# Optimization experiments

Measured on AMD Instinct MI355X. Metric: run time of the kernel, lower is better.

Reference implementation:

```python
import jax, jax.numpy as jnp
import numpy as np
import math

DIM, HEADS = 512, 8
D_K = DIM // HEADS

def setup_inputs() -> dict:
    key = jax.random.key(0)
    ks = jax.random.split(key, 6)
    B, LK, LQ = 16, 2048, 256
    s = 1.0 / math.sqrt(DIM)
    return {
        "L": jax.random.normal(ks[0], (B, LK, DIM), jnp.float32),
        "G": jax.random.normal(ks[1], (B, LQ, DIM), jnp.float32),
        "Wq": jax.random.normal(ks[2], (DIM, DIM), jnp.float32) * s,
        "bq": jnp.zeros((DIM,), jnp.float32),
        "Wo": jax.random.normal(ks[3], (DIM, DIM), jnp.float32) * s,
        "bo": jnp.zeros((DIM,), jnp.float32),
    }

def reference(L, G, Wq, bq, Wo, bo):
    B = G.shape[0]
    # Q projection from global tokens; K,V are raw local features split into heads
    q = (G @ Wq + bq).reshape(B, -1, HEADS, D_K)          # [B, Lq, H, d]
    k = L.reshape(B, -1, HEADS, D_K)                      # [B, Lk, H, d]
    v = k
    # double scaling as in source: / sqrt(d_k) * dim**-0.5
    scale = (D_K ** -0.5) * (DIM ** -0.5)
    dots = jnp.einsum("bqhd,bkhd->bhqk", q, k) * scale    # [B, H, Lq, Lk]
    attn = jax.nn.softmax(dots, axis=-1)
    x = jnp.einsum("bhqk,bkhd->bqhd", attn, v)            # [B, Lq, H, d]
    x = x.reshape(B, -1, HEADS * D_K)
    return x @ Wo + bo
```

## Files before the change

kernel.cpp:

```cpp
#include <hip/hip_runtime.h>

#define KSTR 72

typedef __attribute__((ext_vector_type(8))) short short8;
typedef __attribute__((ext_vector_type(4))) float f32x4;

#define EXP2F(x) __builtin_amdgcn_exp2f(x)

__device__ __forceinline__ unsigned short f2bf(float f) {
    union { float f; unsigned u; } v; v.f = f;
    unsigned r = v.u + 0x7fff + ((v.u >> 16) & 1);
    return (unsigned short)(r >> 16);
}
__device__ __forceinline__ unsigned pk2(float a, float b) {
    return (unsigned)f2bf(a) | ((unsigned)f2bf(b) << 16);
}

__global__ __launch_bounds__(256) void conv_W(const float* __restrict__ Wq,
                                              const float* __restrict__ Wo,
                                              unsigned short* __restrict__ WqF,
                                              unsigned short* __restrict__ WoF) {
    const float* W = blockIdx.y ? Wo : Wq;
    unsigned short* WF = blockIdx.y ? WoF : WqF;
    int g = blockIdx.x * 256 + threadIdx.x;
    int lane = g & 63, ntg = (g >> 6) & 31, kt = g >> 11;
    int c = lane & 15, quad = lane >> 4;
    const float* wp = W + (size_t)(32 * kt + 8 * quad) * 512 + 16 * ntg + c;
    float v[8];
    #pragma unroll
    for (int j = 0; j < 8; j++) v[j] = wp[(size_t)j * 512];
    uint4 u;
    u.x = pk2(v[0], v[1]); u.y = pk2(v[2], v[3]);
    u.z = pk2(v[4], v[5]); u.w = pk2(v[6], v[7]);
    *(uint4*)(WF + (size_t)g * 8) = u;
}

__global__ __launch_bounds__(256) void conv_L(const float* __restrict__ Lmat,
                                              unsigned short* __restrict__ KF,
                                              unsigned short* __restrict__ VF) {
    __shared__ unsigned short KFs[4096];
    __shared__ unsigned short VFs[4096];
    const int blk = blockIdx.x;
    const int t = blk & 31, h = (blk >> 5) & 7, b = blk >> 8;
    const int tid = threadIdx.x;
    const int key = tid & 63, wv = tid >> 6;

    const float* src = Lmat + ((size_t)(b * 2048 + 64 * t + key)) * 512 + 64 * h + 16 * wv;
    float4 a0 = *(const float4*)src;
    float4 a1 = *(const float4*)(src + 4);
    float4 a2 = *(const float4*)(src + 8);
    float4 a3 = *(const float4*)(src + 12);
    float vals[16] = {a0.x, a0.y, a0.z, a0.w, a1.x, a1.y, a1.z, a1.w,
                      a2.x, a2.y, a2.z, a2.w, a3.x, a3.y, a3.z, a3.w};
    #pragma unroll
    for (int i = 0; i < 16; i++) {
        int d = 16 * wv + i;
        unsigned short bv = f2bf(vals[i]);
        KFs[((((key >> 4) * 2 + (d >> 5)) * 64) + ((d >> 3) & 3) * 16 + (key & 15)) * 8 + (d & 7)] = bv;
        VFs[((((d >> 4) * 2 + (key >> 5)) * 64) + ((key >> 3) & 3) * 16 + (d & 15)) * 8 + (key & 7)] = bv;
    }
    __syncthreads();
    size_t gbase = (size_t)blk * 4096 + tid * 16;
    *(uint4*)(KF + gbase)     = *(const uint4*)&KFs[tid * 16];
    *(uint4*)(KF + gbase + 8) = *(const uint4*)&KFs[tid * 16 + 8];
    *(uint4*)(VF + gbase)     = *(const uint4*)&VFs[tid * 16];
    *(uint4*)(VF + gbase + 8) = *(const uint4*)&VFs[tid * 16 + 8];
}

template<bool A_BF16, bool OUT_BF16>
__global__ __launch_bounds__(256, 2) void gemm_direct(const void* __restrict__ Ap,
                                                      const unsigned short* __restrict__ WF,
                                                      const float* __restrict__ bias,
                                                      void* __restrict__ Cp,
                                                      float oscale) {
    const int tid = threadIdx.x;
    const int wv = tid >> 6, lane = tid & 63;
    const int c = lane & 15, quad = lane >> 4;
    const int m0 = blockIdx.x * 64, n0 = blockIdx.y * 64;
    const int row = m0 + 16 * wv + c;

    f32x4 acc[4];
    #pragma unroll
    for (int nt = 0; nt < 4; nt++) acc[nt] = (f32x4){0.f, 0.f, 0.f, 0.f};

    #pragma unroll
    for (int kk = 0; kk < 16; kk++) {
        short8 af;
        if (A_BF16) {
            af = *(const short8*)((const unsigned short*)Ap + (size_t)row * 512 + 32 * kk + 8 * quad);
        } else {
            const float* ap = (const float*)Ap + (size_t)row * 512 + 32 * kk + 8 * quad;
            float4 x0 = *(const float4*)ap;
            float4 x1 = *(const float4*)(ap + 4);
            af[0] = (short)f2bf(x0.x); af[1] = (short)f2bf(x0.y);
            af[2] = (short)f2bf(x0.z); af[3] = (short)f2bf(x0.w);
            af[4] = (short)f2bf(x1.x); af[5] = (short)f2bf(x1.y);
            af[6] = (short)f2bf(x1.z); af[7] = (short)f2bf(x1.w);
        }
        #pragma unroll
        for (int nt = 0; nt < 4; nt++) {
            short8 bf = *(const short8*)(WF +
                (((size_t)kk * 32 + (n0 >> 4) + nt) * 64 + lane) * 8);
            acc[nt] = __builtin_amdgcn_mfma_f32_16x16x32_bf16(af, bf, acc[nt], 0, 0, 0);
        }
    }

    #pragma unroll
    for (int nt = 0; nt < 4; nt++) {
        float bv = bias[n0 + 16 * nt + c];
        #pragma unroll
        for (int r = 0; r < 4; r++) {
            float v = (acc[nt][r] + bv) * oscale;
            size_t idx = (size_t)(m0 + 16 * wv + 4 * quad + r) * 512 + n0 + 16 * nt + c;
            if (OUT_BF16) ((unsigned short*)Cp)[idx] = f2bf(v);
            else          ((float*)Cp)[idx] = v;
        }
    }
}

__global__ __launch_bounds__(256, 2) void attn_frag(const unsigned short* __restrict__ Q,
                                                    const unsigned short* __restrict__ KF,
                                                    const unsigned short* __restrict__ VF,
                                                    unsigned short* __restrict__ X) {
    __shared__ __align__(16) char shm_raw[4 * 64 * 68 * 4];
    unsigned short (*Pw)[4][16 * KSTR] = (unsigned short (*)[4][16 * KSTR])shm_raw;
    float (*Mrg)[64][68] = (float (*)[64][68])shm_raw;

    const int raw = blockIdx.x;
    const int h  = raw & 7;
    const int qt = (raw >> 3) & 3;
    const int b  = raw >> 5;
    const int tid = threadIdx.x;
    const int wv = tid >> 6, lane = tid & 63;
    const int c = lane & 15, quad = lane >> 4;

    short8 qa[4][2];
    #pragma unroll
    for (int g = 0; g < 4; g++) {
        const unsigned short* qsrc =
            Q + ((size_t)(b * 256 + qt * 64 + 16 * g + c)) * 512 + h * 64;
        qa[g][0] = *(const short8*)(qsrc + 8 * quad);
        qa[g][1] = *(const short8*)(qsrc + 32 + 8 * quad);
    }

    short8 ones;
    #pragma unroll
    for (int i = 0; i < 8; i++) ones[i] = (short)0x3F80;

    f32x4 oacc[4][4];
    #pragma unroll
    for (int g = 0; g < 4; g++)
        #pragma unroll
        for (int dt = 0; dt < 4; dt++) oacc[g][dt] = (f32x4){0.f, 0.f, 0.f, 0.f};
    f32x4 lacc[4];
    #pragma unroll
    for (int g = 0; g < 4; g++) lacc[g] = (f32x4){0.f, 0.f, 0.f, 0.f};

    const int swc = (c >> 3) & 1;
    const int swr = (quad >> 1) & 1;

    const unsigned short* kf = KF + ((size_t)((b * 8 + h) * 32)) * 4096 + lane * 8;
    const unsigned short* vf = VF + ((size_t)((b * 8 + h) * 32)) * 4096 + lane * 8;

    for (int i = 0; i < 8; i++) {
        const int T = wv + 4 * i;
        const unsigned short* kt = kf + (size_t)T * 4096;
        const unsigned short* vt = vf + (size_t)T * 4096;
        short8 kbuf[8], vbuf[8];
        #pragma unroll
        for (int f = 0; f < 8; f++) kbuf[f] = *(const short8*)(kt + f * 512);
        #pragma unroll
        for (int f = 0; f < 8; f++) vbuf[f] = *(const short8*)(vt + f * 512);

        #pragma unroll
        for (int g = 0; g < 4; g++) {
            f32x4 sacc[4];
            #pragma unroll
            for (int nt = 0; nt < 4; nt++) sacc[nt] = (f32x4){0.f, 0.f, 0.f, 0.f};
            __builtin_amdgcn_s_setprio(1);
            #pragma unroll
            for (int nt = 0; nt < 4; nt++)
                #pragma unroll
                for (int ks = 0; ks < 2; ks++)
                    sacc[nt] = __builtin_amdgcn_mfma_f32_16x16x32_bf16(
                        qa[g][ks], kbuf[nt * 2 + ks], sacc[nt], 0, 0, 0);
            __builtin_amdgcn_s_setprio(0);
            #pragma unroll
            for (int nt = 0; nt < 4; nt++)
                #pragma unroll
                for (int r = 0; r < 4; r++)
                    Pw[wv][g][(4 * quad + r) * KSTR + ((16 * nt + c) ^ (8 * swr))] =
                        f2bf(EXP2F(sacc[nt][r]));
        }
        #pragma unroll
        for (int g = 0; g < 4; g++) {
            short8 pa0 = *(const short8*)&Pw[wv][g][c * KSTR + 8 * (quad ^ swc)];
            short8 pa1 = *(const short8*)&Pw[wv][g][c * KSTR + 32 + 8 * (quad ^ swc)];
            __builtin_amdgcn_s_setprio(1);
            #pragma unroll
            for (int dt = 0; dt < 4; dt++) {
                oacc[g][dt] = __builtin_amdgcn_mfma_f32_16x16x32_bf16(pa0, vbuf[dt * 2], oacc[g][dt], 0, 0, 0);
                oacc[g][dt] = __builtin_amdgcn_mfma_f32_16x16x32_bf16(pa1, vbuf[dt * 2 + 1], oacc[g][dt], 0, 0, 0);
            }
            lacc[g] = __builtin_amdgcn_mfma_f32_16x16x32_bf16(pa0, ones, lacc[g], 0, 0, 0);
            lacc[g] = __builtin_amdgcn_mfma_f32_16x16x32_bf16(pa1, ones, lacc[g], 0, 0, 0);
            __builtin_amdgcn_s_setprio(0);
        }
    }

    __syncthreads();
    #pragma unroll
    for (int g = 0; g < 4; g++) {
        #pragma unroll
        for (int dt = 0; dt < 4; dt++)
            #pragma unroll
            for (int r = 0; r < 4; r++)
                Mrg[wv][g * 16 + 4 * quad + r][16 * dt + c] = oacc[g][dt][r];
        #pragma unroll
        for (int r = 0; r < 4; r++)
            Mrg[wv][g * 16 + 4 * quad + r][64] = lacc[g][r];
    }
    __syncthreads();
    {
        const int row = 16 * wv + c;
        float sum[16];
        #pragma unroll
        for (int j = 0; j < 16; j++) sum[j] = 0.f;
        float lsum = 0.f;
        #pragma unroll
        for (int ws = 0; ws < 4; ws++) {
            #pragma unroll
            for (int j = 0; j < 16; j++) sum[j] += Mrg[ws][row][16 * quad + j];
            lsum += Mrg[ws][row][64];
        }
        float inv = 1.f / lsum;
        unsigned short us[16];
        #pragma unroll
        for (int j = 0; j < 16; j++) us[j] = f2bf(sum[j] * inv);
        unsigned short* xp =
            X + ((size_t)(b * 256 + qt * 64 + row)) * 512 + h * 64 + 16 * quad;
        *(uint4*)(xp)     = *(uint4*)&us[0];
        *(uint4*)(xp + 8) = *(uint4*)&us[8];
    }
}

extern "C" void kernel_launch(void* const* d_in, const int* in_sizes, int n_in,
                              void* d_out, int out_size, void* d_ws, size_t ws_size,
                              hipStream_t stream) {
    const float* Lmat = (const float*)d_in[0];
    const float* G    = (const float*)d_in[1];
    const float* Wq   = (const float*)d_in[2];
    const float* bq   = (const float*)d_in[3];
    const float* Wo   = (const float*)d_in[4];
    const float* bo   = (const float*)d_in[5];
    float* out = (float*)d_out;

    const float SCe = 0.005524271728019903f * 1.4426950408889634f;
    dim3 gg(64, 8);

    unsigned short* Qws = (unsigned short*)d_ws;
    unsigned short* Xws = Qws + (size_t)2097152;
    unsigned short* WqF = Xws + (size_t)2097152;
    unsigned short* WoF = WqF + (size_t)262144;
    unsigned short* KF  = WoF + (size_t)262144;
    unsigned short* VF  = KF  + (size_t)16777216;

    conv_W<<<dim3(128, 2), 256, 0, stream>>>(Wq, Wo, WqF, WoF);
    conv_L<<<4096, 256, 0, stream>>>(Lmat, KF, VF);
    gemm_direct<false, true><<<gg, 256, 0, stream>>>(G, WqF, bq, Qws, SCe);
    attn_frag<<<512, 256, 0, stream>>>(Qws, KF, VF, Xws);
    gemm_direct<true, false><<<gg, 256, 0, stream>>>(Xws, WoF, bo, out, 1.0f);
}
```

Baseline: 170.1 us.

## Fuse Q projection into attention kernel and merge conversion kernels

Merges the weight and L-conversion kernels into a single launch, and computes the Q projection for each (batch, q-tile, head) inside the attention kernel, staging it in shared memory instead of running a separate GEMM. This drops two kernel launches and the write and re-read of the Q buffer through global memory. In exchange, each attention block now reads a 64x512 slab of G and a 512x64 slice of Wq. The G slab is re-read by all 8 head blocks, so total G traffic grows. The extra shared memory may also affect occupancy.

```diff
diff --git a/kernel.cpp b/kernel.cpp
--- a/kernel.cpp
+++ b/kernel.cpp
@@ -16,33 +16,35 @@
     return (unsigned)f2bf(a) | ((unsigned)f2bf(b) << 16);
 }
 
-__global__ __launch_bounds__(256) void conv_W(const float* __restrict__ Wq,
-                                              const float* __restrict__ Wo,
-                                              unsigned short* __restrict__ WqF,
-                                              unsigned short* __restrict__ WoF) {
-    const float* W = blockIdx.y ? Wo : Wq;
-    unsigned short* WF = blockIdx.y ? WoF : WqF;
-    int g = blockIdx.x * 256 + threadIdx.x;
-    int lane = g & 63, ntg = (g >> 6) & 31, kt = g >> 11;
-    int c = lane & 15, quad = lane >> 4;
-    const float* wp = W + (size_t)(32 * kt + 8 * quad) * 512 + 16 * ntg + c;
-    float v[8];
-    #pragma unroll
-    for (int j = 0; j < 8; j++) v[j] = wp[(size_t)j * 512];
-    uint4 u;
-    u.x = pk2(v[0], v[1]); u.y = pk2(v[2], v[3]);
-    u.z = pk2(v[4], v[5]); u.w = pk2(v[6], v[7]);
-    *(uint4*)(WF + (size_t)g * 8) = u;
-}
-
-__global__ __launch_bounds__(256) void conv_L(const float* __restrict__ Lmat,
-                                              unsigned short* __restrict__ KF,
-                                              unsigned short* __restrict__ VF) {
+__global__ __launch_bounds__(256) void conv_prep(const float* __restrict__ Lmat,
+                                                 const float* __restrict__ Wq,
+                                                 const float* __restrict__ Wo,
+                                                 unsigned short* __restrict__ KF,
+                                                 unsigned short* __restrict__ VF,
+                                                 unsigned short* __restrict__ WqF,
+                                                 unsigned short* __restrict__ WoF) {
+    const int tid = threadIdx.x;
+    if (blockIdx.x >= 4096) {
+        const int idx = blockIdx.x - 4096;
+        const float* W = (idx >> 7) ? Wo : Wq;
+        unsigned short* WF = (idx >> 7) ? WoF : WqF;
+        int g = (idx & 127) * 256 + tid;
+        int lane = g & 63, ntg = (g >> 6) & 31, kt = g >> 11;
+        int c = lane & 15, quad = lane >> 4;
+        const float* wp = W + (size_t)(32 * kt + 8 * quad) * 512 + 16 * ntg + c;
+        float v[8];
+        #pragma unroll
+        for (int j = 0; j < 8; j++) v[j] = wp[(size_t)j * 512];
+        uint4 u;
+        u.x = pk2(v[0], v[1]); u.y = pk2(v[2], v[3]);
+        u.z = pk2(v[4], v[5]); u.w = pk2(v[6], v[7]);
+        *(uint4*)(WF + (size_t)g * 8) = u;
+        return;
+    }
     __shared__ unsigned short KFs[4096];
     __shared__ unsigned short VFs[4096];
     const int blk = blockIdx.x;
     const int t = blk & 31, h = (blk >> 5) & 7, b = blk >> 8;
-    const int tid = threadIdx.x;
     const int key = tid & 63, wv = tid >> 6;
 
     const float* src = Lmat + ((size_t)(b * 2048 + 64 * t + key)) * 512 + 64 * h + 16 * wv;
@@ -118,12 +120,16 @@
     }
 }
 
-__global__ __launch_bounds__(256, 2) void attn_frag(const unsigned short* __restrict__ Q,
+__global__ __launch_bounds__(256, 2) void attn_frag(const float* __restrict__ G,
+                                                    const unsigned short* __restrict__ WqF,
+                                                    const float* __restrict__ bq,
                                                     const unsigned short* __restrict__ KF,
                                                     const unsigned short* __restrict__ VF,
-                                                    unsigned short* __restrict__ X) {
+                                                    unsigned short* __restrict__ X,
+                                                    float SCe) {
     __shared__ __align__(16) char shm_raw[4 * 64 * 68 * 4];
     unsigned short (*Pw)[4][16 * KSTR] = (unsigned short (*)[4][16 * KSTR])shm_raw;
+    unsigned short (*Qs)[72] = (unsigned short (*)[72])(shm_raw + 36864);
     float (*Mrg)[64][68] = (float (*)[64][68])shm_raw;
 
     const int raw = blockIdx.x;
@@ -133,14 +139,46 @@
     const int tid = threadIdx.x;
     const int wv = tid >> 6, lane = tid & 63;
     const int c = lane & 15, quad = lane >> 4;
+    const int n0 = h * 64;
+
+    {
+        f32x4 qacc[4];
+        #pragma unroll
+        for (int nt = 0; nt < 4; nt++) qacc[nt] = (f32x4){0.f, 0.f, 0.f, 0.f};
+        const float* gbase = G + ((size_t)(b * 256 + qt * 64 + 16 * wv + c)) * 512;
+        #pragma unroll
+        for (int kk = 0; kk < 16; kk++) {
+            const float* ap = gbase + 32 * kk + 8 * quad;
+            float4 x0 = *(const float4*)ap;
+            float4 x1 = *(const float4*)(ap + 4);
+            short8 af;
+            af[0] = (short)f2bf(x0.x); af[1] = (short)f2bf(x0.y);
+            af[2] = (short)f2bf(x0.z); af[3] = (short)f2bf(x0.w);
+            af[4] = (short)f2bf(x1.x); af[5] = (short)f2bf(x1.y);
+            af[6] = (short)f2bf(x1.z); af[7] = (short)f2bf(x1.w);
+            #pragma unroll
+            for (int nt = 0; nt < 4; nt++) {
+                short8 bf = *(const short8*)(WqF +
+                    (((size_t)kk * 32 + (n0 >> 4) + nt) * 64 + lane) * 8);
+                qacc[nt] = __builtin_amdgcn_mfma_f32_16x16x32_bf16(af, bf, qacc[nt], 0, 0, 0);
+            }
+        }
+        #pragma unroll
+        for (int nt = 0; nt < 4; nt++) {
+            float bv = bq[n0 + 16 * nt + c];
+            #pragma unroll
+            for (int r = 0; r < 4; r++)
+                Qs[16 * wv + 4 * quad + r][16 * nt + c] =
+                    f2bf((qacc[nt][r] + bv) * SCe);
+        }
+    }
+    __syncthreads();
 
     short8 qa[4][2];
     #pragma unroll
     for (int g = 0; g < 4; g++) {
-        const unsigned short* qsrc =
-            Q + ((size_t)(b * 256 + qt * 64 + 16 * g + c)) * 512 + h * 64;
-        qa[g][0] = *(const short8*)(qsrc + 8 * quad);
-        qa[g][1] = *(const short8*)(qsrc + 32 + 8 * quad);
+        qa[g][0] = *(const short8*)&Qs[16 * g + c][8 * quad];
+        qa[g][1] = *(const short8*)&Qs[16 * g + c][32 + 8 * quad];
     }
 
     short8 ones;
@@ -256,7 +294,6 @@
     float* out = (float*)d_out;
 
     const float SCe = 0.005524271728019903f * 1.4426950408889634f;
-    dim3 gg(64, 8);
 
     unsigned short* Qws = (unsigned short*)d_ws;
     unsigned short* Xws = Qws + (size_t)2097152;
@@ -265,9 +302,7 @@
     unsigned short* KF  = WoF + (size_t)262144;
     unsigned short* VF  = KF  + (size_t)16777216;
 
-    conv_W<<<dim3(128, 2), 256, 0, stream>>>(Wq, Wo, WqF, WoF);
-    conv_L<<<4096, 256, 0, stream>>>(Lmat, KF, VF);
-    gemm_direct<false, true><<<gg, 256, 0, stream>>>(G, WqF, bq, Qws, SCe);
-    attn_frag<<<512, 256, 0, stream>>>(Qws, KF, VF, Xws);
-    gemm_direct<true, false><<<gg, 256, 0, stream>>>(Xws, WoF, bo, out, 1.0f);
-}
+    conv_prep<<<4352, 256, 0, stream>>>(Lmat, Wq, Wo, KF, VF, WqF, WoF);
+    attn_frag<<<512, 256, 0, stream>>>(G, WqF, bq, KF, VF, Xws, SCe);
+    gemm_direct<true, false><<<dim3(64, 8), 256, 0, stream>>>(Xws, WoF, bo, out, 1.0f);
+}
```

After: 164.3 us. 1.04x faster.
